# Kernel optimization log

Measured on AMD Instinct MI355X. Metric: run time of the kernel, lower is better.

Reference implementation:

```python
import jax, jax.numpy as jnp
import numpy as np

MUL = 128                      # multiplicity (channels) per irrep of x1
INV_SQRT3 = float(1.0 / np.sqrt(3.0))  # normalized CG for 1x1->0 (dot)
INV_SQRT2 = float(1.0 / np.sqrt(2.0))  # normalized CG for 1x1->1 (cross)


def setup_inputs() -> dict:
    key = jax.random.key(0)
    k1, k2, k3 = jax.random.split(key, 3)
    N = 50000
    # x1: 128x0e + 128x1o  -> dim 128 + 128*3 = 512
    x1 = jax.random.normal(k1, (N, 512), dtype=jnp.float32)
    # x2: 1x0e + 1x1o -> dim 4 (spherical harmonics l=0,1)
    x2 = jax.random.normal(k2, (N, 4), dtype=jnp.float32)
    # per-edge weights, 'uvu' mode: one weight per (instruction, channel) = 5*128
    weights = jax.random.normal(k3, (N, 640), dtype=jnp.float32)
    return {"x1": x1, "x2": x2, "weights": weights}


def _cg_tensor_product(x1, x2, weights):
    """Loop-unrolled Clebsch-Gordan tensor product, 'uvu' connection mode.

    x1: [N, 512]  = 128x0e + 128x1o
    x2: [N, 4]    = 1x0e + 1x1o
    weights: [N, 640] = 5 instructions x 128 channels
    out: [N, 1408] = 128x0e + 128x1o + 128x1o + 128x0e + 128x1e
    """
    N = x1.shape[0]
    x1_0 = x1[:, :MUL]                       # [N, U]    scalars (l=0)
    x1_1 = x1[:, MUL:].reshape(N, MUL, 3)    # [N, U, 3] vectors (l=1)
    x2_0 = x2[:, 0]                          # [N]       scalar
    x2_1 = x2[:, 1:4]                        # [N, 3]    vector
    w = weights.reshape(N, 5, MUL)           # [N, 5, U]

    # instruction 0: 0e x 0e -> 0e   (scalar product)
    out0 = w[:, 0] * x1_0 * x2_0[:, None]                                  # [N, U]
    # instruction 1: 0e x 1o -> 1o   (scalar * vector)
    out1 = w[:, 1][:, :, None] * x1_0[:, :, None] * x2_1[:, None, :]       # [N, U, 3]
    # instruction 2: 1o x 0e -> 1o   (vector * scalar)
    out2 = w[:, 2][:, :, None] * x1_1 * x2_0[:, None, None]                # [N, U, 3]
    # instruction 3: 1o x 1o -> 0e   (dot / sqrt(3))
    dot = jnp.einsum('num,nm->nu', x1_1, x2_1)                             # [N, U]
    out3 = w[:, 3] * dot * INV_SQRT3
    # instruction 4: 1o x 1o -> 1e   (cross / sqrt(2))
    crs = jnp.cross(x1_1, x2_1[:, None, :])                                # [N, U, 3]
    out4 = w[:, 4][:, :, None] * crs * INV_SQRT2

    return jnp.concatenate(
        [out0, out1.reshape(N, -1), out2.reshape(N, -1), out3, out4.reshape(N, -1)],
        axis=1,
    )


def reference(x1, x2, weights):
    return _cg_tensor_product(x1, x2, weights)
```

## Files before the change

### kernel.cpp

```cpp
#include <hip/hip_runtime.h>

#define MUL 128

__global__ __launch_bounds__(256) void cg_tp_kernel(
    const float* __restrict__ x1,
    const float* __restrict__ x2,
    const float* __restrict__ wts,
    float* __restrict__ out,
    int N)
{
    constexpr float INV_SQRT3 = 0.57735026918962576451f;
    constexpr float INV_SQRT2 = 0.70710678118654752440f;

    int gid = blockIdx.x * blockDim.x + threadIdx.x;
    int total = N * MUL;
    if (gid >= total) return;

    int row = gid >> 7;
    int u   = gid & 127;

    const float* x1r  = x1  + (size_t)row * 512;
    const float* x2r  = x2  + (size_t)row * 4;
    const float* wr   = wts + (size_t)row * 640;
    float*       outr = out + (size_t)row * 1408;

    float x10 = x1r[u];
    float a0 = x1r[128 + u * 3 + 0];
    float a1 = x1r[128 + u * 3 + 1];
    float a2 = x1r[128 + u * 3 + 2];
    float s  = x2r[0];
    float b0 = x2r[1];
    float b1 = x2r[2];
    float b2 = x2r[3];
    float w0 = wr[0 * MUL + u];
    float w1 = wr[1 * MUL + u];
    float w2 = wr[2 * MUL + u];
    float w3 = wr[3 * MUL + u];
    float w4 = wr[4 * MUL + u];

    outr[u] = w0 * x10 * s;

    float w1x = w1 * x10;
    outr[128 + u * 3 + 0] = w1x * b0;
    outr[128 + u * 3 + 1] = w1x * b1;
    outr[128 + u * 3 + 2] = w1x * b2;

    float w2s = w2 * s;
    outr[512 + u * 3 + 0] = w2s * a0;
    outr[512 + u * 3 + 1] = w2s * a1;
    outr[512 + u * 3 + 2] = w2s * a2;

    float dot = a0 * b0 + a1 * b1 + a2 * b2;
    outr[896 + u] = w3 * dot * INV_SQRT3;

    float c0 = a1 * b2 - a2 * b1;
    float c1 = a2 * b0 - a0 * b2;
    float c2 = a0 * b1 - a1 * b0;
    float w4s = w4 * INV_SQRT2;
    outr[1024 + u * 3 + 0] = w4s * c0;
    outr[1024 + u * 3 + 1] = w4s * c1;
    outr[1024 + u * 3 + 2] = w4s * c2;
}

extern "C" void kernel_launch(void* const* d_in, const int* in_sizes, int n_in,
                              void* d_out, int out_size, void* d_ws, size_t ws_size,
                              hipStream_t stream)
{
    const float* x1  = (const float*)d_in[0];
    const float* x2  = (const float*)d_in[1];
    const float* wts = (const float*)d_in[2];
    float* out = (float*)d_out;

    int N = in_sizes[0] / 512;
    int total = N * MUL;
    int block = 256;
    int grid = (total + block - 1) / block;
    cg_tp_kernel<<<grid, block, 0, stream>>>(x1, x2, wts, out, N);
}
```

Measured before the change: 97.75 us.

## Stage rows through shared memory for vectorized coalesced loads and stores

Each block now handles four rows, copies x1, weights and x2 into shared memory with float4 loads, computes the tensor product into a shared output buffer, then writes the output back with float4 stores. This replaces the strided 3-component global accesses with wide contiguous transfers to use memory bandwidth better. In exchange it needs about 41 KB of LDS per block, which lowers occupancy, and it adds two barriers that serialize the load, compute and store phases within each block.

New measurement: 109.5 us. 1.12x slower.

```diff
diff --git a/kernel.cpp b/kernel.cpp
--- a/kernel.cpp
+++ b/kernel.cpp
@@ -1,8 +1,10 @@
 #include <hip/hip_runtime.h>
 
 #define MUL 128
+#define RPB 4
+#define BLOCK 256
 
-__global__ __launch_bounds__(256) void cg_tp_kernel(
+__global__ __launch_bounds__(BLOCK) void cg_tp_kernel(
     const float* __restrict__ x1,
     const float* __restrict__ x2,
     const float* __restrict__ wts,
@@ -12,54 +14,80 @@
     constexpr float INV_SQRT3 = 0.57735026918962576451f;
     constexpr float INV_SQRT2 = 0.70710678118654752440f;
 
-    int gid = blockIdx.x * blockDim.x + threadIdx.x;
-    int total = N * MUL;
-    if (gid >= total) return;
+    __shared__ float s_x1[RPB][512];
+    __shared__ float s_w [RPB][640];
+    __shared__ float s_x2[RPB][4];
+    __shared__ float s_out[RPB][1408];
 
-    int row = gid >> 7;
-    int u   = gid & 127;
+    const int tid  = threadIdx.x;
+    const int row0 = blockIdx.x * RPB;
+    const int nrows = min(RPB, N - row0);
 
-    const float* x1r  = x1  + (size_t)row * 512;
-    const float* x2r  = x2  + (size_t)row * 4;
-    const float* wr   = wts + (size_t)row * 640;
-    float*       outr = out + (size_t)row * 1408;
+    {
+        const float4* g = (const float4*)(x1 + (size_t)row0 * 512);
+        float4* s = (float4*)&s_x1[0][0];
+        for (int i = tid; i < nrows * 128; i += BLOCK) s[i] = g[i];
+    }
+    {
+        const float4* g = (const float4*)(wts + (size_t)row0 * 640);
+        float4* s = (float4*)&s_w[0][0];
+        for (int i = tid; i < nrows * 160; i += BLOCK) s[i] = g[i];
+    }
+    {
+        const float4* g = (const float4*)(x2 + (size_t)row0 * 4);
+        float4* s = (float4*)&s_x2[0][0];
+        if (tid < nrows) s[tid] = g[tid];
+    }
+    __syncthreads();
 
-    float x10 = x1r[u];
-    float a0 = x1r[128 + u * 3 + 0];
-    float a1 = x1r[128 + u * 3 + 1];
-    float a2 = x1r[128 + u * 3 + 2];
-    float s  = x2r[0];
-    float b0 = x2r[1];
-    float b1 = x2r[2];
-    float b2 = x2r[3];
-    float w0 = wr[0 * MUL + u];
-    float w1 = wr[1 * MUL + u];
-    float w2 = wr[2 * MUL + u];
-    float w3 = wr[3 * MUL + u];
-    float w4 = wr[4 * MUL + u];
+    for (int j = tid; j < nrows * MUL; j += BLOCK) {
+        const int r = j >> 7;
+        const int u = j & 127;
 
-    outr[u] = w0 * x10 * s;
+        float x10 = s_x1[r][u];
+        float a0  = s_x1[r][128 + 3 * u + 0];
+        float a1  = s_x1[r][128 + 3 * u + 1];
+        float a2  = s_x1[r][128 + 3 * u + 2];
+        float sc  = s_x2[r][0];
+        float b0  = s_x2[r][1];
+        float b1  = s_x2[r][2];
+        float b2  = s_x2[r][3];
+        float w0  = s_w[r][0 * MUL + u];
+        float w1  = s_w[r][1 * MUL + u];
+        float w2  = s_w[r][2 * MUL + u];
+        float w3  = s_w[r][3 * MUL + u];
+        float w4  = s_w[r][4 * MUL + u];
 
-    float w1x = w1 * x10;
-    outr[128 + u * 3 + 0] = w1x * b0;
-    outr[128 + u * 3 + 1] = w1x * b1;
-    outr[128 + u * 3 + 2] = w1x * b2;
+        s_out[r][u] = w0 * x10 * sc;
 
-    float w2s = w2 * s;
-    outr[512 + u * 3 + 0] = w2s * a0;
-    outr[512 + u * 3 + 1] = w2s * a1;
-    outr[512 + u * 3 + 2] = w2s * a2;
+        float w1x = w1 * x10;
+        s_out[r][128 + 3 * u + 0] = w1x * b0;
+        s_out[r][128 + 3 * u + 1] = w1x * b1;
+        s_out[r][128 + 3 * u + 2] = w1x * b2;
 
-    float dot = a0 * b0 + a1 * b1 + a2 * b2;
-    outr[896 + u] = w3 * dot * INV_SQRT3;
+        float w2s = w2 * sc;
+        s_out[r][512 + 3 * u + 0] = w2s * a0;
+        s_out[r][512 + 3 * u + 1] = w2s * a1;
+        s_out[r][512 + 3 * u + 2] = w2s * a2;
 
-    float c0 = a1 * b2 - a2 * b1;
-    float c1 = a2 * b0 - a0 * b2;
-    float c2 = a0 * b1 - a1 * b0;
-    float w4s = w4 * INV_SQRT2;
-    outr[1024 + u * 3 + 0] = w4s * c0;
-    outr[1024 + u * 3 + 1] = w4s * c1;
-    outr[1024 + u * 3 + 2] = w4s * c2;
+        float dot = a0 * b0 + a1 * b1 + a2 * b2;
+        s_out[r][896 + u] = w3 * dot * INV_SQRT3;
+
+        float c0 = a1 * b2 - a2 * b1;
+        float c1 = a2 * b0 - a0 * b2;
+        float c2 = a0 * b1 - a1 * b0;
+        float w4s = w4 * INV_SQRT2;
+        s_out[r][1024 + 3 * u + 0] = w4s * c0;
+        s_out[r][1024 + 3 * u + 1] = w4s * c1;
+        s_out[r][1024 + 3 * u + 2] = w4s * c2;
+    }
+    __syncthreads();
+
+    {
+        float4* g = (float4*)(out + (size_t)row0 * 1408);
+        const float4* s = (const float4*)&s_out[0][0];
+        for (int i = tid; i < nrows * 352; i += BLOCK) g[i] = s[i];
+    }
 }
 
 extern "C" void kernel_launch(void* const* d_in, const int* in_sizes, int n_in,
@@ -72,8 +100,6 @@
     float* out = (float*)d_out;
 
     int N = in_sizes[0] / 512;
-    int total = N * MUL;
-    int block = 256;
-    int grid = (total + block - 1) / block;
-    cg_tp_kernel<<<grid, block, 0, stream>>>(x1, x2, wts, out, N);
+    int grid = (N + RPB - 1) / RPB;
+    cg_tp_kernel<<<grid, BLOCK, 0, stream>>>(x1, x2, wts, out, N);
 }
```

## Map one thread per output element with XCD-aware block remapping and nontemporal stores

Applied to the files above, without the earlier changes.

Restructures the kernel so each thread produces a single output element. Each row gets two blocks of 704 threads, so stores are fully coalesced instead of stride-3 per channel. Block IDs are remapped so consecutive rows land on the same XCD, which improves L2 locality for the repeated reads of x1 and weights, and outputs use nontemporal stores. The cost is divergent branches per output segment, integer division by 3, and redundant input loads across threads that rely on the cache.

After: 172.6 us. +76.6%, slower.

```diff
diff --git a/kernel.cpp b/kernel.cpp
--- a/kernel.cpp
+++ b/kernel.cpp
@@ -1,65 +1,63 @@
 #include <hip/hip_runtime.h>
 
-#define MUL 128
+#define BLOCK 704
 
-__global__ __launch_bounds__(256) void cg_tp_kernel(
+__global__ __launch_bounds__(BLOCK) void cg_tp_kernel(
     const float* __restrict__ x1,
     const float* __restrict__ x2,
     const float* __restrict__ wts,
     float* __restrict__ out,
-    int N)
+    int N, int nblocks)
 {
     constexpr float INV_SQRT3 = 0.57735026918962576451f;
     constexpr float INV_SQRT2 = 0.70710678118654752440f;
 
-    int gid = blockIdx.x * blockDim.x + threadIdx.x;
-    int total = N * MUL;
-    if (gid >= total) return;
+    int b   = blockIdx.x;
+    int q   = nblocks >> 3, rr = nblocks & 7;
+    int xcd = b & 7, idx = b >> 3;
+    int Lb  = (xcd < rr ? xcd * (q + 1) : rr * (q + 1) + (xcd - rr) * q) + idx;
 
-    int row = gid >> 7;
-    int u   = gid & 127;
+    int row = Lb >> 1;
+    if (row >= N) return;
+    int j = (Lb & 1) * BLOCK + (int)threadIdx.x;
 
-    const float* x1r  = x1  + (size_t)row * 512;
-    const float* x2r  = x2  + (size_t)row * 4;
-    const float* wr   = wts + (size_t)row * 640;
-    float*       outr = out + (size_t)row * 1408;
+    const float* x1r = x1  + (size_t)row * 512;
+    const float* wr  = wts + (size_t)row * 640;
+    float4 X2 = *(const float4*)(x2 + (size_t)row * 4);
+    float s = X2.x, b0 = X2.y, b1 = X2.z, b2 = X2.w;
 
-    float x10 = x1r[u];
-    float a0 = x1r[128 + u * 3 + 0];
-    float a1 = x1r[128 + u * 3 + 1];
-    float a2 = x1r[128 + u * 3 + 2];
-    float s  = x2r[0];
-    float b0 = x2r[1];
-    float b1 = x2r[2];
-    float b2 = x2r[3];
-    float w0 = wr[0 * MUL + u];
-    float w1 = wr[1 * MUL + u];
-    float w2 = wr[2 * MUL + u];
-    float w3 = wr[3 * MUL + u];
-    float w4 = wr[4 * MUL + u];
+    float o;
+    if (j < 128) {
+        o = wr[j] * x1r[j] * s;
+    } else if (j < 512) {
+        unsigned e = (unsigned)(j - 128);
+        unsigned u = e / 3u;
+        unsigned c = e - 3u * u;
+        float bb = (c == 0u) ? b0 : ((c == 1u) ? b1 : b2);
+        o = wr[128 + u] * x1r[u] * bb;
+    } else if (j < 896) {
+        unsigned e = (unsigned)(j - 512);
+        unsigned u = e / 3u;
+        o = wr[256 + u] * s * x1r[128 + e];
+    } else if (j < 1024) {
+        unsigned u = (unsigned)(j - 896);
+        const float* a = x1r + 128 + 3 * u;
+        float dot = a[0] * b0 + a[1] * b1 + a[2] * b2;
+        o = wr[384 + u] * dot * INV_SQRT3;
+    } else {
+        unsigned e = (unsigned)(j - 1024);
+        unsigned u = e / 3u;
+        unsigned c = e - 3u * u;
+        const float* a = x1r + 128 + 3 * u;
+        float a0 = a[0], a1 = a[1], a2 = a[2];
+        float cr0 = a1 * b2 - a2 * b1;
+        float cr1 = a2 * b0 - a0 * b2;
+        float cr2 = a0 * b1 - a1 * b0;
+        float cc = (c == 0u) ? cr0 : ((c == 1u) ? cr1 : cr2);
+        o = wr[512 + u] * cc * INV_SQRT2;
+    }
 
-    outr[u] = w0 * x10 * s;
-
-    float w1x = w1 * x10;
-    outr[128 + u * 3 + 0] = w1x * b0;
-    outr[128 + u * 3 + 1] = w1x * b1;
-    outr[128 + u * 3 + 2] = w1x * b2;
-
-    float w2s = w2 * s;
-    outr[512 + u * 3 + 0] = w2s * a0;
-    outr[512 + u * 3 + 1] = w2s * a1;
-    outr[512 + u * 3 + 2] = w2s * a2;
-
-    float dot = a0 * b0 + a1 * b1 + a2 * b2;
-    outr[896 + u] = w3 * dot * INV_SQRT3;
-
-    float c0 = a1 * b2 - a2 * b1;
-    float c1 = a2 * b0 - a0 * b2;
-    float c2 = a0 * b1 - a1 * b0;
-    float w4s = w4 * INV_SQRT2;
-    outr[1024 + u * 3 + 0] = w4s * c0;
-    outr[1024 + u * 3 + 1] = w4s * c1;
-    outr[1024 + u * 3 + 2] = w4s * c2;
+    __builtin_nontemporal_store(o, out + (size_t)row * 1408 + j);
 }
 
 extern "C" void kernel_launch(void* const* d_in, const int* in_sizes, int n_in,
@@ -72,8 +70,6 @@
     float* out = (float*)d_out;
 
     int N = in_sizes[0] / 512;
-    int total = N * MUL;
-    int block = 256;
-    int grid = (total + block - 1) / block;
-    cg_tp_kernel<<<grid, block, 0, stream>>>(x1, x2, wts, out, N);
+    int nblocks = 2 * N;
+    cg_tp_kernel<<<nblocks, BLOCK, 0, stream>>>(x1, x2, wts, out, N, nblocks);
 }
```
